# Kernel tuning notes

Measured on AMD Instinct MI355X. Metric: run time of the kernel, lower is better.

The kernel has to match this reference:

```python
import jax, jax.numpy as jnp
import numpy as np

N_TOKENS = 65536
HIDDEN = 1024
N_EXPERTS = 64
EPS = 1e-12  # matches F.normalize default eps
NEG_BIG = float(jnp.finfo(jnp.bfloat16).max)  # -torch.finfo(bfloat16).max sentinel


def setup_inputs() -> dict:
    key = jax.random.key(0)
    k1, k2 = jax.random.split(key)
    x = jax.random.normal(k1, (N_TOKENS, HIDDEN), dtype=jnp.float32)
    sim_matrix = jax.random.normal(k2, (HIDDEN, N_EXPERTS), dtype=jnp.float32)  # nn.Parameter(randn)
    gates = jnp.zeros((N_EXPERTS,), dtype=jnp.float32)  # nn.Parameter(zeros)
    return {"x": x, "sim_matrix": sim_matrix, "gates": gates}


def _l2norm(v, axis):
    n = jnp.sqrt(jnp.sum(v * v, axis=axis, keepdims=True))
    return v / jnp.maximum(n, EPS)


def reference(x, sim_matrix, gates):
    # cosine-similarity logits: [N, E]
    logits = jnp.matmul(_l2norm(x, -1), _l2norm(sim_matrix, 0))
    thr = jax.nn.sigmoid(gates)                      # [E]
    pre_activation_logits = logits - thr             # [N, E]
    gated = jax.nn.relu(pre_activation_logits)
    # STE: forward hard 0/1, backward identity
    hard = (gated > 0).astype(x.dtype)
    activation_mask = gated + jax.lax.stop_gradient(hard - gated)
    # topk fallback for rows with zero active experts (vectorized scatter)
    inactive = jnp.sum(hard, axis=1) == 0            # [N]
    k_fallback = N_EXPERTS // 2
    _, topk_idx = jax.lax.top_k(logits, k_fallback)  # [N, k]
    rows = jnp.arange(x.shape[0])
    fb = jnp.zeros_like(logits).at[rows[:, None], topk_idx].set(1.0)
    activation_mask = jnp.where(inactive[:, None], fb, activation_mask)
    # masked softmax over active experts
    masked = jnp.where(activation_mask > 0, gated, -NEG_BIG)
    active_expert_probs = jax.nn.softmax(masked, axis=-1)
    return active_expert_probs, pre_activation_logits, activation_mask
```

## Files before the change

### kernel.cpp

```cpp
#include <hip/hip_runtime.h>
#include <math.h>

#define N_TOK   65536
#define HID     1024
#define NEXP    64
#define EPSF    1e-12f

__global__ __launch_bounds__(256) void prep_kernel(const float* __restrict__ sim,
                                                   const float* __restrict__ gates,
                                                   float* __restrict__ ws) {
    __shared__ float partial[4][64];
    int e = threadIdx.x & 63;
    int q = threadIdx.x >> 6;
    float s = 0.f;
    for (int h = q * 256; h < q * 256 + 256; ++h) {
        float v = sim[h * NEXP + e];
        s += v * v;
    }
    partial[q][e] = s;
    __syncthreads();
    if (threadIdx.x < 64) {
        float ss = partial[0][e] + partial[1][e] + partial[2][e] + partial[3][e];
        ws[e] = 1.0f / fmaxf(sqrtf(ss), EPSF);
        ws[64 + e] = 1.0f / (1.0f + expf(-gates[e]));
    }
}

__global__ __launch_bounds__(256) void prep2n_kernel(const float* __restrict__ sim,
                                                     const float* __restrict__ ws_ro,
                                                     float* __restrict__ wn) {
    int idx = blockIdx.x * 256 + threadIdx.x;
    wn[idx] = sim[idx] * ws_ro[idx & 63];
}

__global__ __launch_bounds__(128) void gate_v8_kernel(const float* __restrict__ x,
                                                      const float* __restrict__ wn,
                                                      const float* __restrict__ prep,
                                                      float* __restrict__ out) {
    __shared__ __align__(16) float smem[8832];
    float* ss_part = smem + 8704;

    const int tid  = threadIdx.x;
    const int lane = tid & 63;
    const int wv   = tid >> 6;
    const int tg   = lane >> 3;
    const int eg   = lane & 7;
    const int e0   = eg * 8;
    const int tbase = blockIdx.x * 64;
    const int kbase = wv * 512;

    float* xsw = smem + wv * 4352;

    const float4* xq4 = (const float4*)(x + (size_t)(tbase + lane) * HID + kbase);

    float acc[8][8];
#pragma unroll
    for (int t = 0; t < 8; ++t)
#pragma unroll
        for (int e = 0; e < 8; ++e) acc[t][e] = 0.f;
    float ss = 0.f;

    {
        float4 st[8];
#pragma unroll
        for (int q = 0; q < 8; ++q) st[q] = xq4[q];
#pragma unroll
        for (int q = 0; q < 8; ++q) {
            ss = fmaf(st[q].x, st[q].x, ss);
            ss = fmaf(st[q].y, st[q].y, ss);
            ss = fmaf(st[q].z, st[q].z, ss);
            ss = fmaf(st[q].w, st[q].w, ss);
            xsw[(q * 4 + 0) * 68 + lane] = st[q].x;
            xsw[(q * 4 + 1) * 68 + lane] = st[q].y;
            xsw[(q * 4 + 2) * 68 + lane] = st[q].z;
            xsw[(q * 4 + 3) * 68 + lane] = st[q].w;
        }
    }

#define FMA8x8(XA, XB, WA, WB)                                              \
    do {                                                                    \
        const float xv_[8] = { XA.x, XA.y, XA.z, XA.w, XB.x, XB.y, XB.z, XB.w }; \
        const float wv_[8] = { WA.x, WA.y, WA.z, WA.w, WB.x, WB.y, WB.z, WB.w }; \
        _Pragma("unroll")                                                   \
        for (int t_ = 0; t_ < 8; ++t_)                                      \
            _Pragma("unroll")                                               \
            for (int e_ = 0; e_ < 8; ++e_)                                  \
                acc[t_][e_] = fmaf(xv_[t_], wv_[e_], acc[t_][e_]);          \
    } while (0)

#pragma unroll 1
    for (int c = 0; c < 16; ++c) {
        float4 st[8];
        if (c < 15) {
#pragma unroll
            for (int q = 0; q < 8; ++q) st[q] = xq4[(c + 1) * 8 + q];
        }

        const float* xb = xsw + (c & 1) * 2176;
        const float* wbase = wn + (size_t)(kbase + c * 32) * NEXP + e0;

        float4 a0 = *(const float4*)(wbase);
        float4 b0 = *(const float4*)(wbase + 4);
        float4 a1 = *(const float4*)(wbase + 64);
        float4 b1 = *(const float4*)(wbase + 68);

#pragma unroll 4
        for (int k = 0; k < 32; k += 2) {
            float4 na0, nb0, na1, nb1;
            if (k + 2 < 32) {
                na0 = *(const float4*)(wbase + (k + 2) * 64);
                nb0 = *(const float4*)(wbase + (k + 2) * 64 + 4);
                na1 = *(const float4*)(wbase + (k + 3) * 64);
                nb1 = *(const float4*)(wbase + (k + 3) * 64 + 4);
            }
            const float4 xa0 = *(const float4*)&xb[k * 68 + tg * 8];
            const float4 xb0 = *(const float4*)&xb[k * 68 + tg * 8 + 4];
            const float4 xa1 = *(const float4*)&xb[(k + 1) * 68 + tg * 8];
            const float4 xb1 = *(const float4*)&xb[(k + 1) * 68 + tg * 8 + 4];
            FMA8x8(xa0, xb0, a0, b0);
            FMA8x8(xa1, xb1, a1, b1);
            a0 = na0; b0 = nb0; a1 = na1; b1 = nb1;
        }

        if (c < 15) {
            float* xn = xsw + ((c + 1) & 1) * 2176;
#pragma unroll
            for (int q = 0; q < 8; ++q) {
                ss = fmaf(st[q].x, st[q].x, ss);
                ss = fmaf(st[q].y, st[q].y, ss);
                ss = fmaf(st[q].z, st[q].z, ss);
                ss = fmaf(st[q].w, st[q].w, ss);
                xn[(q * 4 + 0) * 68 + lane] = st[q].x;
                xn[(q * 4 + 1) * 68 + lane] = st[q].y;
                xn[(q * 4 + 2) * 68 + lane] = st[q].z;
                xn[(q * 4 + 3) * 68 + lane] = st[q].w;
            }
        }
    }
#undef FMA8x8

    ss_part[wv * 64 + lane] = ss;

    if (wv == 1) {
        float* plane = smem + 4352;
#pragma unroll
        for (int j = 0; j < 8; ++j) {
            float* p = &plane[(tg * 8 + j) * 64 + e0];
            *(float4*)(p)     = make_float4(acc[j][0], acc[j][1], acc[j][2], acc[j][3]);
            *(float4*)(p + 4) = make_float4(acc[j][4], acc[j][5], acc[j][6], acc[j][7]);
        }
    }
    __syncthreads();

    if (wv == 0) {
        const float* plane = smem + 4352;
#pragma unroll
        for (int j = 0; j < 8; ++j) {
            const float* p = &plane[(tg * 8 + j) * 64 + e0];
            float4 p0 = *(const float4*)(p);
            float4 p1 = *(const float4*)(p + 4);
            acc[j][0] += p0.x; acc[j][1] += p0.y; acc[j][2] += p0.z; acc[j][3] += p0.w;
            acc[j][4] += p1.x; acc[j][5] += p1.y; acc[j][6] += p1.z; acc[j][7] += p1.w;
            float* lg = &smem[(tg * 8 + j) * 68 + e0];
            *(float4*)(lg)     = make_float4(acc[j][0], acc[j][1], acc[j][2], acc[j][3]);
            *(float4*)(lg + 4) = make_float4(acc[j][4], acc[j][5], acc[j][6], acc[j][7]);
        }
    }
    __syncthreads();

    float thr[8];
#pragma unroll
    for (int i = 0; i < 8; ++i) thr[i] = prep[64 + e0 + i];

    const size_t out_pre  = (size_t)N_TOK * NEXP;
    const size_t out_mask = 2 * (size_t)N_TOK * NEXP;

#pragma unroll
    for (int j = 0; j < 4; ++j) {
        const int tl = wv * 32 + tg * 4 + j;
        const int t  = tbase + tl;
        const float sst = ss_part[tl] + ss_part[64 + tl];
        const float inv = 1.0f / fmaxf(sqrtf(sst), EPSF);

        float4 l0 = *(const float4*)&smem[tl * 68 + e0];
        float4 l1 = *(const float4*)&smem[tl * 68 + e0 + 4];
        float logit[8] = { l0.x * inv, l0.y * inv, l0.z * inv, l0.w * inv,
                           l1.x * inv, l1.y * inv, l1.z * inv, l1.w * inv };
        float pre[8], gated[8];
        int active[8];
        int myact = 0;
#pragma unroll
        for (int i = 0; i < 8; ++i) {
            pre[i]   = logit[i] - thr[i];
            gated[i] = fmaxf(pre[i], 0.f);
            active[i] = pre[i] > 0.f;
            myact += active[i];
        }
        int rowact = myact;
        rowact += __shfl_xor(rowact, 1, 8);
        rowact += __shfl_xor(rowact, 2, 8);
        rowact += __shfl_xor(rowact, 4, 8);

        float probs[8], mask[8];
        if (rowact > 0) {
            float m = -INFINITY;
#pragma unroll
            for (int i = 0; i < 8; ++i) m = fmaxf(m, active[i] ? gated[i] : -INFINITY);
            m = fmaxf(m, __shfl_xor(m, 1, 8));
            m = fmaxf(m, __shfl_xor(m, 2, 8));
            m = fmaxf(m, __shfl_xor(m, 4, 8));
            float s = 0.f;
#pragma unroll
            for (int i = 0; i < 8; ++i) {
                float ev = active[i] ? expf(gated[i] - m) : 0.f;
                probs[i] = ev; s += ev;
            }
            s += __shfl_xor(s, 1, 8);
            s += __shfl_xor(s, 2, 8);
            s += __shfl_xor(s, 4, 8);
            float rs = 1.0f / s;
#pragma unroll
            for (int i = 0; i < 8; ++i) {
                probs[i] *= rs;
                mask[i] = active[i] ? 1.f : 0.f;
            }
        } else {
            unsigned key[8];
#pragma unroll
            for (int i = 0; i < 8; ++i) {
                unsigned u = __float_as_uint(logit[i]);
                key[i] = (u & 0x80000000u) ? ~u : (u | 0x80000000u);
            }
            unsigned cand = 0u;
            for (int bit = 31; bit >= 0; --bit) {
                unsigned test = cand | (1u << bit);
                int c = 0;
#pragma unroll
                for (int i = 0; i < 8; ++i) c += (key[i] >= test);
                c += __shfl_xor(c, 1, 8);
                c += __shfl_xor(c, 2, 8);
                c += __shfl_xor(c, 4, 8);
                if (c >= 32) cand = test;
            }
            int cgt = 0;
#pragma unroll
            for (int i = 0; i < 8; ++i) cgt += (key[i] > cand);
            cgt += __shfl_xor(cgt, 1, 8);
            cgt += __shfl_xor(cgt, 2, 8);
            cgt += __shfl_xor(cgt, 4, 8);
            int need_eq = 32 - cgt;

            int eqc = 0;
#pragma unroll
            for (int i = 0; i < 8; ++i) eqc += (key[i] == cand);
            int scan = eqc, tmp;
            tmp = __shfl_up(scan, 1, 8); if (eg >= 1) scan += tmp;
            tmp = __shfl_up(scan, 2, 8); if (eg >= 2) scan += tmp;
            tmp = __shfl_up(scan, 4, 8); if (eg >= 4) scan += tmp;
            int run = scan - eqc;
#pragma unroll
            for (int i = 0; i < 8; ++i) {
                int sel = (key[i] > cand) || ((key[i] == cand) && (run < need_eq));
                run += (key[i] == cand);
                mask[i]  = sel ? 1.f : 0.f;
                probs[i] = sel ? 0.03125f : 0.f;
            }
        }

        const size_t row = (size_t)t * NEXP + e0;
        *(float4*)&out[row]                = make_float4(probs[0], probs[1], probs[2], probs[3]);
        *(float4*)&out[row + 4]            = make_float4(probs[4], probs[5], probs[6], probs[7]);
        *(float4*)&out[out_pre + row]      = make_float4(pre[0], pre[1], pre[2], pre[3]);
        *(float4*)&out[out_pre + row + 4]  = make_float4(pre[4], pre[5], pre[6], pre[7]);
        *(float4*)&out[out_mask + row]     = make_float4(mask[0], mask[1], mask[2], mask[3]);
        *(float4*)&out[out_mask + row + 4] = make_float4(mask[4], mask[5], mask[6], mask[7]);
    }
}

#define TOKB    128
#define KC      64
#define XPAD    65

__global__ __launch_bounds__(256) void gate_kernel_fb(const float* __restrict__ x,
                                                      const float* __restrict__ sim,
                                                      const float* __restrict__ prep,
                                                      float* __restrict__ out) {
    __shared__ float x_lds[TOKB][XPAD];
    __shared__ float w_lds[KC][NEXP];
    __shared__ float ss_lds[TOKB];
    __shared__ float invcol[NEXP];
    __shared__ float thr_s[NEXP];

    const int tid = threadIdx.x;
    const int base_t = blockIdx.x * TOKB;

    if (tid < NEXP) { invcol[tid] = prep[tid]; thr_s[tid] = prep[64 + tid]; }
    if (tid < TOKB) ss_lds[tid] = 0.f;

    const int g_e = tid & 7;
    const int g_t = tid >> 3;
    const int e0 = g_e * 8;
    const int t0 = g_t * 4;

    const int lt = tid >> 4;
    const int lk = (tid & 15) * 4;

    float acc[4][8];
#pragma unroll
    for (int j = 0; j < 4; ++j)
#pragma unroll
        for (int i = 0; i < 8; ++i) acc[j][i] = 0.f;

    for (int kc = 0; kc < HID; kc += KC) {
        __syncthreads();
#pragma unroll
        for (int it = 0; it < 4; ++it) {
            int flat4 = it * 256 + tid;
            int k = flat4 >> 4;
            int e = (flat4 & 15) * 4;
            float4 v = *(const float4*)&sim[(size_t)(kc + k) * NEXP + e];
            v.x *= invcol[e]; v.y *= invcol[e + 1]; v.z *= invcol[e + 2]; v.w *= invcol[e + 3];
            *(float4*)&w_lds[k][e] = v;
        }
#pragma unroll
        for (int it = 0; it < 8; ++it) {
            int t = it * 16 + lt;
            float4 v = *(const float4*)&x[(size_t)(base_t + t) * HID + kc + lk];
            x_lds[t][lk + 0] = v.x; x_lds[t][lk + 1] = v.y;
            x_lds[t][lk + 2] = v.z; x_lds[t][lk + 3] = v.w;
            float s4 = v.x * v.x + v.y * v.y + v.z * v.z + v.w * v.w;
            s4 += __shfl_xor(s4, 1, 16);
            s4 += __shfl_xor(s4, 2, 16);
            s4 += __shfl_xor(s4, 4, 16);
            s4 += __shfl_xor(s4, 8, 16);
            if ((tid & 15) == 0) ss_lds[t] += s4;
        }
        __syncthreads();
#pragma unroll 8
        for (int k = 0; k < KC; ++k) {
            float x0 = x_lds[t0 + 0][k];
            float x1 = x_lds[t0 + 1][k];
            float x2 = x_lds[t0 + 2][k];
            float x3 = x_lds[t0 + 3][k];
            float4 w0 = *(const float4*)&w_lds[k][e0];
            float4 w1 = *(const float4*)&w_lds[k][e0 + 4];
            float wv[8] = { w0.x, w0.y, w0.z, w0.w, w1.x, w1.y, w1.z, w1.w };
#pragma unroll
            for (int i = 0; i < 8; ++i) {
                acc[0][i] += x0 * wv[i];
                acc[1][i] += x1 * wv[i];
                acc[2][i] += x2 * wv[i];
                acc[3][i] += x3 * wv[i];
            }
        }
    }

    const size_t out_pre  = (size_t)N_TOK * NEXP;
    const size_t out_mask = 2 * (size_t)N_TOK * NEXP;

#pragma unroll
    for (int j = 0; j < 4; ++j) {
        int t = t0 + j;
        float inv = 1.0f / fmaxf(sqrtf(ss_lds[t]), EPSF);
        float logit[8], pre[8], gated[8];
        int active[8];
        int myact = 0;
#pragma unroll
        for (int i = 0; i < 8; ++i) {
            logit[i] = acc[j][i] * inv;
            pre[i]   = logit[i] - thr_s[e0 + i];
            gated[i] = fmaxf(pre[i], 0.f);
            active[i] = pre[i] > 0.f;
            myact += active[i];
        }
        int rowact = myact;
        rowact += __shfl_xor(rowact, 1, 8);
        rowact += __shfl_xor(rowact, 2, 8);
        rowact += __shfl_xor(rowact, 4, 8);

        float probs[8], mask[8];
        if (rowact > 0) {
            float m = -INFINITY;
#pragma unroll
            for (int i = 0; i < 8; ++i) m = fmaxf(m, active[i] ? gated[i] : -INFINITY);
            m = fmaxf(m, __shfl_xor(m, 1, 8));
            m = fmaxf(m, __shfl_xor(m, 2, 8));
            m = fmaxf(m, __shfl_xor(m, 4, 8));
            float s = 0.f;
#pragma unroll
            for (int i = 0; i < 8; ++i) {
                float ev = active[i] ? expf(gated[i] - m) : 0.f;
                probs[i] = ev; s += ev;
            }
            s += __shfl_xor(s, 1, 8);
            s += __shfl_xor(s, 2, 8);
            s += __shfl_xor(s, 4, 8);
            float rs = 1.0f / s;
#pragma unroll
            for (int i = 0; i < 8; ++i) {
                probs[i] *= rs;
                mask[i] = active[i] ? 1.f : 0.f;
            }
        } else {
            unsigned key[8];
#pragma unroll
            for (int i = 0; i < 8; ++i) {
                unsigned u = __float_as_uint(logit[i]);
                key[i] = (u & 0x80000000u) ? ~u : (u | 0x80000000u);
            }
            unsigned cand = 0u;
            for (int bit = 31; bit >= 0; --bit) {
                unsigned test = cand | (1u << bit);
                int c = 0;
#pragma unroll
                for (int i = 0; i < 8; ++i) c += (key[i] >= test);
                c += __shfl_xor(c, 1, 8);
                c += __shfl_xor(c, 2, 8);
                c += __shfl_xor(c, 4, 8);
                if (c >= 32) cand = test;
            }
            int cgt = 0;
#pragma unroll
            for (int i = 0; i < 8; ++i) cgt += (key[i] > cand);
            cgt += __shfl_xor(cgt, 1, 8);
            cgt += __shfl_xor(cgt, 2, 8);
            cgt += __shfl_xor(cgt, 4, 8);
            int need_eq = 32 - cgt;

            int eqc = 0;
#pragma unroll
            for (int i = 0; i < 8; ++i) eqc += (key[i] == cand);
            int scan = eqc, tmp;
            tmp = __shfl_up(scan, 1, 8); if (g_e >= 1) scan += tmp;
            tmp = __shfl_up(scan, 2, 8); if (g_e >= 2) scan += tmp;
            tmp = __shfl_up(scan, 4, 8); if (g_e >= 4) scan += tmp;
            int run = scan - eqc;
#pragma unroll
            for (int i = 0; i < 8; ++i) {
                int sel = (key[i] > cand) || ((key[i] == cand) && (run < need_eq));
                run += (key[i] == cand);
                mask[i]  = sel ? 1.f : 0.f;
                probs[i] = sel ? 0.03125f : 0.f;
            }
        }

        size_t row = (size_t)(base_t + t) * NEXP + e0;
        *(float4*)&out[row]                = make_float4(probs[0], probs[1], probs[2], probs[3]);
        *(float4*)&out[row + 4]            = make_float4(probs[4], probs[5], probs[6], probs[7]);
        *(float4*)&out[out_pre + row]      = make_float4(pre[0], pre[1], pre[2], pre[3]);
        *(float4*)&out[out_pre + row + 4]  = make_float4(pre[4], pre[5], pre[6], pre[7]);
        *(float4*)&out[out_mask + row]     = make_float4(mask[0], mask[1], mask[2], mask[3]);
        *(float4*)&out[out_mask + row + 4] = make_float4(mask[4], mask[5], mask[6], mask[7]);
    }
}

extern "C" void kernel_launch(void* const* d_in, const int* in_sizes, int n_in,
                              void* d_out, int out_size, void* d_ws, size_t ws_size,
                              hipStream_t stream) {
    (void)in_sizes; (void)n_in; (void)out_size;
    const float* x     = (const float*)d_in[0];
    const float* sim   = (const float*)d_in[1];
    const float* gates = (const float*)d_in[2];
    float* out = (float*)d_out;
    float* ws  = (float*)d_ws;

    hipLaunchKernelGGL(prep_kernel, dim3(1), dim3(256), 0, stream, sim, gates, ws);

    const size_t need = 512 + (size_t)HID * NEXP * sizeof(float);
    if (ws_size >= need) {
        float* wn = ws + 128;
        hipLaunchKernelGGL(prep2n_kernel, dim3(HID * NEXP / 256), dim3(256), 0, stream,
                           sim, ws, wn);
        hipLaunchKernelGGL(gate_v8_kernel, dim3(N_TOK / 64), dim3(128), 0, stream,
                           x, wn, ws, out);
    } else {
        hipLaunchKernelGGL(gate_kernel_fb, dim3(N_TOK / TOKB), dim3(256), 0, stream,
                           x, sim, ws, out);
    }
}
```

Baseline: 183.6 us.

## Split hidden-dim reduction across four waves per block instead of two

The gating kernel now runs 256 threads per block, with each of four waves handling a 256-wide slice of the hidden dimension, where before two waves each handled 512. The partial logits are combined pairwise through shared memory, and the sum-of-squares partials are merged across four waves. The epilogue is spread over all four waves, two tokens per thread group. This aims to raise the number of waves in flight to hide global-load latency, at the cost of an extra reduction stage, one more barrier and more LDS traffic.

```diff
diff --git a/kernel.cpp b/kernel.cpp
--- a/kernel.cpp
+++ b/kernel.cpp
@@ -33,11 +33,11 @@
     wn[idx] = sim[idx] * ws_ro[idx & 63];
 }
 
-__global__ __launch_bounds__(128) void gate_v8_kernel(const float* __restrict__ x,
+__global__ __launch_bounds__(256) void gate_v9_kernel(const float* __restrict__ x,
                                                       const float* __restrict__ wn,
                                                       const float* __restrict__ prep,
                                                       float* __restrict__ out) {
-    __shared__ __align__(16) float smem[8832];
+    __shared__ __align__(16) float smem[8960];
     float* ss_part = smem + 8704;
 
     const int tid  = threadIdx.x;
@@ -47,11 +47,10 @@
     const int eg   = lane & 7;
     const int e0   = eg * 8;
     const int tbase = blockIdx.x * 64;
-    const int kbase = wv * 512;
-
-    float* xsw = smem + wv * 4352;
-
-    const float4* xq4 = (const float4*)(x + (size_t)(tbase + lane) * HID + kbase);
+
+    float* xsw = smem + wv * 2176;
+
+    const float4* xq4 = (const float4*)(x + (size_t)(tbase + lane) * HID + wv * 256);
 
     float acc[8][8];
 #pragma unroll
@@ -61,11 +60,11 @@
     float ss = 0.f;
 
     {
-        float4 st[8];
-#pragma unroll
-        for (int q = 0; q < 8; ++q) st[q] = xq4[q];
-#pragma unroll
-        for (int q = 0; q < 8; ++q) {
+        float4 st[4];
+#pragma unroll
+        for (int q = 0; q < 4; ++q) st[q] = xq4[q];
+#pragma unroll
+        for (int q = 0; q < 4; ++q) {
             ss = fmaf(st[q].x, st[q].x, ss);
             ss = fmaf(st[q].y, st[q].y, ss);
             ss = fmaf(st[q].z, st[q].z, ss);
@@ -90,14 +89,14 @@
 
 #pragma unroll 1
     for (int c = 0; c < 16; ++c) {
-        float4 st[8];
+        float4 st[4];
         if (c < 15) {
 #pragma unroll
-            for (int q = 0; q < 8; ++q) st[q] = xq4[(c + 1) * 8 + q];
-        }
-
-        const float* xb = xsw + (c & 1) * 2176;
-        const float* wbase = wn + (size_t)(kbase + c * 32) * NEXP + e0;
+            for (int q = 0; q < 4; ++q) st[q] = xq4[(c + 1) * 4 + q];
+        }
+
+        const float* xb = xsw + (c & 1) * 1088;
+        const float* wbase = wn + (size_t)(wv * 256 + c * 16) * NEXP + e0;
 
         float4 a0 = *(const float4*)(wbase);
         float4 b0 = *(const float4*)(wbase + 4);
@@ -105,9 +104,9 @@
         float4 b1 = *(const float4*)(wbase + 68);
 
 #pragma unroll 4
-        for (int k = 0; k < 32; k += 2) {
+        for (int k = 0; k < 16; k += 2) {
             float4 na0, nb0, na1, nb1;
-            if (k + 2 < 32) {
+            if (k + 2 < 16) {
                 na0 = *(const float4*)(wbase + (k + 2) * 64);
                 nb0 = *(const float4*)(wbase + (k + 2) * 64 + 4);
                 na1 = *(const float4*)(wbase + (k + 3) * 64);
@@ -123,9 +122,9 @@
         }
 
         if (c < 15) {
-            float* xn = xsw + ((c + 1) & 1) * 2176;
-#pragma unroll
-            for (int q = 0; q < 8; ++q) {
+            float* xn = xsw + ((c + 1) & 1) * 1088;
+#pragma unroll
+            for (int q = 0; q < 4; ++q) {
                 ss = fmaf(st[q].x, st[q].x, ss);
                 ss = fmaf(st[q].y, st[q].y, ss);
                 ss = fmaf(st[q].z, st[q].z, ss);
@@ -140,30 +139,29 @@
 #undef FMA8x8
 
     ss_part[wv * 64 + lane] = ss;
-
-    if (wv == 1) {
-        float* plane = smem + 4352;
+    __syncthreads();
+
+    if (wv < 2) {
+        float* reg = smem + wv * 4352;
 #pragma unroll
         for (int j = 0; j < 8; ++j) {
-            float* p = &plane[(tg * 8 + j) * 64 + e0];
+            float* p = &reg[(tg * 8 + j) * 68 + e0];
             *(float4*)(p)     = make_float4(acc[j][0], acc[j][1], acc[j][2], acc[j][3]);
             *(float4*)(p + 4) = make_float4(acc[j][4], acc[j][5], acc[j][6], acc[j][7]);
         }
     }
     __syncthreads();
-
-    if (wv == 0) {
-        const float* plane = smem + 4352;
+    if (wv >= 2) {
+        float* reg = smem + (wv - 2) * 4352;
 #pragma unroll
         for (int j = 0; j < 8; ++j) {
-            const float* p = &plane[(tg * 8 + j) * 64 + e0];
+            float* p = &reg[(tg * 8 + j) * 68 + e0];
             float4 p0 = *(const float4*)(p);
             float4 p1 = *(const float4*)(p + 4);
-            acc[j][0] += p0.x; acc[j][1] += p0.y; acc[j][2] += p0.z; acc[j][3] += p0.w;
-            acc[j][4] += p1.x; acc[j][5] += p1.y; acc[j][6] += p1.z; acc[j][7] += p1.w;
-            float* lg = &smem[(tg * 8 + j) * 68 + e0];
-            *(float4*)(lg)     = make_float4(acc[j][0], acc[j][1], acc[j][2], acc[j][3]);
-            *(float4*)(lg + 4) = make_float4(acc[j][4], acc[j][5], acc[j][6], acc[j][7]);
+            p0.x += acc[j][0]; p0.y += acc[j][1]; p0.z += acc[j][2]; p0.w += acc[j][3];
+            p1.x += acc[j][4]; p1.y += acc[j][5]; p1.z += acc[j][6]; p1.w += acc[j][7];
+            *(float4*)(p)     = p0;
+            *(float4*)(p + 4) = p1;
         }
     }
     __syncthreads();
@@ -174,18 +172,25 @@
 
     const size_t out_pre  = (size_t)N_TOK * NEXP;
     const size_t out_mask = 2 * (size_t)N_TOK * NEXP;
-
-#pragma unroll
-    for (int j = 0; j < 4; ++j) {
-        const int tl = wv * 32 + tg * 4 + j;
+    const float* regA = smem;
+    const float* regB = smem + 4352;
+
+#pragma unroll
+    for (int j = 0; j < 2; ++j) {
+        const int tl = wv * 16 + tg * 2 + j;
         const int t  = tbase + tl;
-        const float sst = ss_part[tl] + ss_part[64 + tl];
+        const float sst = (ss_part[tl] + ss_part[64 + tl])
+                        + (ss_part[128 + tl] + ss_part[192 + tl]);
         const float inv = 1.0f / fmaxf(sqrtf(sst), EPSF);
 
-        float4 l0 = *(const float4*)&smem[tl * 68 + e0];
-        float4 l1 = *(const float4*)&smem[tl * 68 + e0 + 4];
-        float logit[8] = { l0.x * inv, l0.y * inv, l0.z * inv, l0.w * inv,
-                           l1.x * inv, l1.y * inv, l1.z * inv, l1.w * inv };
+        float4 aA0 = *(const float4*)&regA[tl * 68 + e0];
+        float4 aA1 = *(const float4*)&regA[tl * 68 + e0 + 4];
+        float4 aB0 = *(const float4*)&regB[tl * 68 + e0];
+        float4 aB1 = *(const float4*)&regB[tl * 68 + e0 + 4];
+        float logit[8] = { (aA0.x + aB0.x) * inv, (aA0.y + aB0.y) * inv,
+                           (aA0.z + aB0.z) * inv, (aA0.w + aB0.w) * inv,
+                           (aA1.x + aB1.x) * inv, (aA1.y + aB1.y) * inv,
+                           (aA1.z + aB1.z) * inv, (aA1.w + aB1.w) * inv };
         float pre[8], gated[8];
         int active[8];
         int myact = 0;
@@ -471,7 +476,7 @@
         float* wn = ws + 128;
         hipLaunchKernelGGL(prep2n_kernel, dim3(HID * NEXP / 256), dim3(256), 0, stream,
                            sim, ws, wn);
-        hipLaunchKernelGGL(gate_v8_kernel, dim3(N_TOK / 64), dim3(128), 0, stream,
+        hipLaunchKernelGGL(gate_v9_kernel, dim3(N_TOK / 64), dim3(256), 0, stream,
                            x, wn, ws, out);
     } else {
         hipLaunchKernelGGL(gate_kernel_fb, dim3(N_TOK / TOKB), dim3(256), 0, stream,
```

After: 174.7 us. 4.9% less time.
